# Kernel tuning notes

Measured on AMD Instinct MI355X. Metric: run time of the kernel, lower is better.

Reference implementation:

```python
import jax, jax.numpy as jnp
import numpy as np

T = 16384
D_IN = 512
D_HID = 512
D_OUT = 512


def setup_inputs() -> dict:
    key = jax.random.key(0)
    ks = jax.random.split(key, 7)
    s_in = 1.0 / np.sqrt(D_IN)
    s_hid = 1.0 / np.sqrt(D_HID)
    xs = jax.random.normal(ks[0], (T, D_IN), dtype=jnp.float32)
    Wz = jax.random.uniform(ks[1], (D_HID, D_IN), jnp.float32, -s_in, s_in)
    bz = jax.random.uniform(ks[2], (D_HID,), jnp.float32, -s_in, s_in)
    Wh = jax.random.uniform(ks[3], (D_HID, D_IN), jnp.float32, -s_in, s_in)
    bh = jax.random.uniform(ks[4], (D_HID,), jnp.float32, -s_in, s_in)
    Wo = jax.random.uniform(ks[5], (D_OUT, D_HID), jnp.float32, -s_hid, s_hid)
    bo = jax.random.uniform(ks[6], (D_OUT,), jnp.float32, -s_hid, s_hid)
    return {"xs": xs, "Wz": Wz, "bz": bz, "Wh": Wh, "bh": bh, "Wo": Wo, "bo": bo}


def _combine(first, second):
    a0, b0 = first
    a1, b1 = second
    return (a0 * a1, a1 * b0 + b1)


def reference(xs, Wz, bz, Wh, bh, Wo, bo):
    # gates and candidate hidden states: [T, H]
    zs = jax.nn.sigmoid(xs @ Wz.T + bz)
    hs = xs @ Wh.T + bh
    # prepend identity element (a=1, b=0) for the h_0 = 0 initial state
    a = jnp.concatenate([jnp.ones((1, zs.shape[1]), zs.dtype), 1.0 - zs], axis=0)
    b = jnp.concatenate([jnp.zeros((1, zs.shape[1]), zs.dtype), zs * hs], axis=0)
    _, states = jax.lax.associative_scan(_combine, (a, b))  # [T+1, H]
    return states[1:] @ Wo.T + bo  # [T, D_OUT]
```

## Files before the change

### kernel.cpp

```cpp
#include <hip/hip_runtime.h>
#include <hip/hip_bf16.h>
#include <cstdint>
#include <cmath>

#define T_SEQ 16384
#define DMODEL 512
#define NCHUNK 512
#define LCHUNK 32
#define W_N    (DMODEL * DMODEL)
#define N4_W   (W_N / 4)
#define N4_W3  (3 * N4_W)
#define N4_X   (T_SEQ * DMODEL / 4)
#define N4_ALL (N4_W3 + N4_X)
#define NTILE  8

typedef __bf16 bf16x8 __attribute__((ext_vector_type(8)));
typedef float  f32x4  __attribute__((ext_vector_type(4)));

using bf16 = __hip_bfloat16;

__device__ __forceinline__ void load_lds16(const void* g, void* l) {
    __builtin_amdgcn_global_load_lds((const __attribute__((address_space(1))) void*)g,
                                     (__attribute__((address_space(3))) void*)l,
                                     16, 0, 0);
}

__device__ __forceinline__ unsigned short f2bf(float f) {
    union { float f; unsigned u; } v; v.f = f;
    const unsigned r = (v.u + 0x7FFFu + ((v.u >> 16) & 1u)) >> 16;
    return (unsigned short)r;
}
__device__ __forceinline__ float bf2f(unsigned short u) {
    union { unsigned u; float f; } v; v.u = ((unsigned)u) << 16;
    return v.f;
}

__device__ __forceinline__ void comb(float& A, float& B, float fA, float fB,
                                     float sA, float sB) {
    A = fA * sA;
    B = sA * fB + sB;
}

__global__ __launch_bounds__(256) void k_convert(
    const float* __restrict__ xs,
    const float* __restrict__ Wz, const float* __restrict__ Wh,
    const float* __restrict__ Wo,
    bf16* __restrict__ xs_c, bf16* __restrict__ Wz_c,
    bf16* __restrict__ Wh_c, bf16* __restrict__ Wo_c)
{
    const int i = blockIdx.x * 256 + threadIdx.x;
    if (i >= N4_ALL) return;
    const float* src; bf16* dst; int o;
    if (i < N4_W3) {
        const int w = i >> 16; o = i & 65535;
        src = (w == 0) ? Wz : (w == 1) ? Wh : Wo;
        dst = (w == 0) ? Wz_c : (w == 1) ? Wh_c : Wo_c;
    } else {
        o = i - N4_W3; src = xs; dst = xs_c;
    }
    const float4 v = ((const float4*)src)[o];
    ushort4 r;
    r.x = f2bf(v.x); r.y = f2bf(v.y); r.z = f2bf(v.z); r.w = f2bf(v.w);
    ((ushort4*)dst)[o] = r;
}

__global__ __launch_bounds__(512, 2) void gemm_zh(
    const bf16* __restrict__ xs_c, const bf16* __restrict__ Wz, const float* __restrict__ bz,
    const bf16* __restrict__ Wh, const float* __restrict__ bh,
    unsigned int* __restrict__ ab_ws,
    float* __restrict__ ABagg)
{
    __shared__ __bf16 As[2][2][256 * 32];
    __shared__ __bf16 Zs[2][2][128 * 32];
    __shared__ __bf16 Hs[2][2][128 * 32];

    const int tid  = threadIdx.x;
    const int bm   = blockIdx.x;
    const int bn   = blockIdx.y;
    const int lane = tid & 63;
    const int wave = tid >> 6;
    const int wm   = wave >> 1;
    const int wn   = wave & 1;
    const int quad = lane >> 4;
    const int col  = lane & 15;

    f32x4 accz[4][4], acch[4][4];
    #pragma unroll
    for (int i = 0; i < 4; ++i)
        #pragma unroll
        for (int j = 0; j < 4; ++j) {
            accz[i][j] = (f32x4){0.f, 0.f, 0.f, 0.f};
            acch[i][j] = (f32x4){0.f, 0.f, 0.f, 0.f};
        }

    const int srow = tid >> 2;
    const int wq   = (tid & 3) ^ ((tid >> 3) & 3);
    const bf16* ag = xs_c + (size_t)(bm * 256 + srow) * DMODEL + wq * 8;
    const bf16* zg = Wz   + (size_t)(bn * 128 + srow) * DMODEL + wq * 8;
    const bf16* hg = Wh   + (size_t)(bn * 128 + srow) * DMODEL + wq * 8;

    const int fq = quad ^ ((col >> 1) & 3);
    int offA[4], offB[4];
    #pragma unroll
    for (int i = 0; i < 4; ++i) {
        offA[i] = (wm * 64 + i * 16 + col) * 32 + fq * 8;
        offB[i] = (wn * 64 + i * 16 + col) * 32 + fq * 8;
    }

    auto STAGE_HALF = [&](int t, int h) {
        const int b  = t & 1;
        const int ko = t * 64 + h * 32;
        load_lds16(ag + ko,                          &As[b][h][tid * 8]);
        load_lds16(ag + (size_t)128 * DMODEL + ko,   &As[b][h][(512 + tid) * 8]);
        load_lds16(zg + ko,                          &Zs[b][h][tid * 8]);
        load_lds16(hg + ko,                          &Hs[b][h][tid * 8]);
    };

    STAGE_HALF(0, 0); STAGE_HALF(0, 1);

    #pragma unroll
    for (int t = 0; t < NTILE; ++t) {
        const int b = t & 1;
        bf16x8 af[4], zf[4], hf[4];

        asm volatile("s_waitcnt vmcnt(4)" ::: "memory");
        __builtin_amdgcn_s_barrier();
        __builtin_amdgcn_sched_barrier(0);
        if (t + 1 < NTILE) STAGE_HALF(t + 1, 0);
        #pragma unroll
        for (int i = 0; i < 4; ++i) {
            af[i] = *(const bf16x8*)&As[b][0][offA[i]];
            zf[i] = *(const bf16x8*)&Zs[b][0][offB[i]];
        }
        __builtin_amdgcn_s_setprio(1);
        #pragma unroll
        for (int i = 0; i < 4; ++i)
            #pragma unroll
            for (int j = 0; j < 4; ++j)
                accz[i][j] = __builtin_amdgcn_mfma_f32_16x16x32_bf16(af[i], zf[j], accz[i][j], 0, 0, 0);
        __builtin_amdgcn_s_setprio(0);

        #pragma unroll
        for (int j = 0; j < 4; ++j)
            hf[j] = *(const bf16x8*)&Hs[b][0][offB[j]];
        __builtin_amdgcn_s_setprio(1);
        #pragma unroll
        for (int i = 0; i < 4; ++i)
            #pragma unroll
            for (int j = 0; j < 4; ++j)
                acch[i][j] = __builtin_amdgcn_mfma_f32_16x16x32_bf16(af[i], hf[j], acch[i][j], 0, 0, 0);
        __builtin_amdgcn_s_setprio(0);

        if (t + 1 < NTILE) {
            asm volatile("s_waitcnt vmcnt(4)" ::: "memory");
        } else {
            asm volatile("s_waitcnt vmcnt(0)" ::: "memory");
        }
        __builtin_amdgcn_s_barrier();
        __builtin_amdgcn_sched_barrier(0);
        if (t + 1 < NTILE) STAGE_HALF(t + 1, 1);
        #pragma unroll
        for (int i = 0; i < 4; ++i) {
            af[i] = *(const bf16x8*)&As[b][1][offA[i]];
            zf[i] = *(const bf16x8*)&Zs[b][1][offB[i]];
        }
        __builtin_amdgcn_s_setprio(1);
        #pragma unroll
        for (int i = 0; i < 4; ++i)
            #pragma unroll
            for (int j = 0; j < 4; ++j)
                accz[i][j] = __builtin_amdgcn_mfma_f32_16x16x32_bf16(af[i], zf[j], accz[i][j], 0, 0, 0);
        __builtin_amdgcn_s_setprio(0);

        #pragma unroll
        for (int j = 0; j < 4; ++j)
            hf[j] = *(const bf16x8*)&Hs[b][1][offB[j]];
        __builtin_amdgcn_s_setprio(1);
        #pragma unroll
        for (int i = 0; i < 4; ++i)
            #pragma unroll
            for (int j = 0; j < 4; ++j)
                acch[i][j] = __builtin_amdgcn_mfma_f32_16x16x32_bf16(af[i], hf[j], acch[i][j], 0, 0, 0);
        __builtin_amdgcn_s_setprio(0);
    }

    const int c_lo = bm * 8 + wm * 2;
    #pragma unroll
    for (int j = 0; j < 4; ++j) {
        const int n = bn * 128 + wn * 64 + j * 16 + col;
        const float bzv = bz[n];
        const float bhv = bh[n];
        float cA[4], cB[4];
        #pragma unroll
        for (int i = 0; i < 4; ++i) {
            const int mbase = bm * 256 + wm * 64 + i * 16 + quad * 4;
            float A = 1.f, B = 0.f;
            #pragma unroll
            for (int r = 0; r < 4; ++r) {
                const float zpre = accz[i][j][r] + bzv;
                const float hpre = acch[i][j][r] + bhv;
                const float z = 1.f / (1.f + __expf(-zpre));
                const float a = 1.f - z;
                const float b = z * hpre;
                const size_t idx = (size_t)(mbase + r) * DMODEL + n;
                ab_ws[idx] = (unsigned)f2bf(a) | ((unsigned)f2bf(b) << 16);
                A = a * A;
                B = a * B + b;
            }
            cA[i] = A; cB[i] = B;
        }
        #pragma unroll
        for (int i = 0; i < 4; ++i) {
            float pA = __shfl_xor(cA[i], 16);
            float pB = __shfl_xor(cB[i], 16);
            const bool hi1 = quad & 1;
            comb(cA[i], cB[i], hi1 ? pA : cA[i], hi1 ? pB : cB[i],
                               hi1 ? cA[i] : pA, hi1 ? cB[i] : pB);
            pA = __shfl_xor(cA[i], 32);
            pB = __shfl_xor(cB[i], 32);
            const bool hi2 = quad >> 1;
            comb(cA[i], cB[i], hi2 ? pA : cA[i], hi2 ? pB : cB[i],
                               hi2 ? cA[i] : pA, hi2 ? cB[i] : pB);
        }
        float Alo, Blo, Ahi, Bhi;
        comb(Alo, Blo, cA[0], cB[0], cA[1], cB[1]);
        comb(Ahi, Bhi, cA[2], cB[2], cA[3], cB[3]);
        if (quad == 0) {
            *(float4*)&ABagg[((size_t)n * NCHUNK + c_lo) * 2] =
                make_float4(Alo, Blo, Ahi, Bhi);
        }
    }
}

__global__ __launch_bounds__(512) void scan_p2(
    const float* __restrict__ ABagg, float* __restrict__ HpreT)
{
    const int h = blockIdx.x;
    const int c = threadIdx.x;
    __shared__ float sA[NCHUNK], sB[NCHUNK];

    const float2 v = ((const float2*)ABagg)[(size_t)h * NCHUNK + c];
    float A = v.x;
    float B = v.y;
    sA[c] = A; sB[c] = B;
    __syncthreads();

    for (int off = 1; off < NCHUNK; off <<= 1) {
        float pA = 1.f, pB = 0.f;
        if (c >= off) { pA = sA[c - off]; pB = sB[c - off]; }
        __syncthreads();
        const float nB = A * pB + B;
        const float nA = A * pA;
        A = nA; B = nB;
        sA[c] = A; sB[c] = B;
        __syncthreads();
    }
    const float hp = (c == 0) ? 0.f : sB[c - 1];
    HpreT[(size_t)h * NCHUNK + c] = hp;
}

__global__ __launch_bounds__(256) void scan_p3(
    const unsigned int* __restrict__ ab_ws, const float* __restrict__ HpreT,
    unsigned short* __restrict__ states)
{
    const int tid = threadIdx.x;
    const int c   = blockIdx.x;
    const int ch  = blockIdx.y * 256 + tid;
    float H = HpreT[(size_t)ch * NCHUNK + c];
    const size_t base = (size_t)(c * LCHUNK) * DMODEL + ch;
    #pragma unroll 8
    for (int i = 0; i < LCHUNK; ++i) {
        const unsigned u = ab_ws[base + (size_t)i * DMODEL];
        const float a = bf2f((unsigned short)(u & 0xFFFFu));
        const float b = bf2f((unsigned short)(u >> 16));
        H = a * H + b;
        states[base + (size_t)i * DMODEL] = f2bf(H);
    }
}

__global__ __launch_bounds__(512, 2) void gemm_out(
    const bf16* __restrict__ states, const bf16* __restrict__ Wo, const float* __restrict__ bo,
    float* __restrict__ out)
{
    __shared__ __bf16 As[2][2][256 * 32];
    __shared__ __bf16 Bs[2][2][128 * 32];

    const int tid  = threadIdx.x;
    const int bm   = blockIdx.x;
    const int bn   = blockIdx.y;
    const int lane = tid & 63;
    const int wave = tid >> 6;
    const int wm   = wave >> 1;
    const int wn   = wave & 1;
    const int quad = lane >> 4;
    const int col  = lane & 15;

    f32x4 acc[4][4];
    #pragma unroll
    for (int i = 0; i < 4; ++i)
        #pragma unroll
        for (int j = 0; j < 4; ++j)
            acc[i][j] = (f32x4){0.f, 0.f, 0.f, 0.f};

    const int srow = tid >> 2;
    const int wq   = (tid & 3) ^ ((tid >> 3) & 3);
    const bf16* ag = states + (size_t)(bm * 256 + srow) * DMODEL + wq * 8;
    const bf16* bg = Wo     + (size_t)(bn * 128 + srow) * DMODEL + wq * 8;

    const int fq = quad ^ ((col >> 1) & 3);
    int offA[4], offB[4];
    #pragma unroll
    for (int i = 0; i < 4; ++i) {
        offA[i] = (wm * 64 + i * 16 + col) * 32 + fq * 8;
        offB[i] = (wn * 64 + i * 16 + col) * 32 + fq * 8;
    }

    auto STAGE_HALF = [&](int t, int h) {
        const int b  = t & 1;
        const int ko = t * 64 + h * 32;
        load_lds16(ag + ko,                        &As[b][h][tid * 8]);
        load_lds16(ag + (size_t)128 * DMODEL + ko, &As[b][h][(512 + tid) * 8]);
        load_lds16(bg + ko,                        &Bs[b][h][tid * 8]);
    };

    STAGE_HALF(0, 0); STAGE_HALF(0, 1);

    #pragma unroll
    for (int t = 0; t < NTILE; ++t) {
        const int b = t & 1;
        bf16x8 af[4], bf[4];

        asm volatile("s_waitcnt vmcnt(3)" ::: "memory");
        __builtin_amdgcn_s_barrier();
        __builtin_amdgcn_sched_barrier(0);
        if (t + 1 < NTILE) STAGE_HALF(t + 1, 0);
        #pragma unroll
        for (int i = 0; i < 4; ++i) {
            af[i] = *(const bf16x8*)&As[b][0][offA[i]];
            bf[i] = *(const bf16x8*)&Bs[b][0][offB[i]];
        }
        __builtin_amdgcn_s_setprio(1);
        #pragma unroll
        for (int i = 0; i < 4; ++i)
            #pragma unroll
            for (int j = 0; j < 4; ++j)
                acc[i][j] = __builtin_amdgcn_mfma_f32_16x16x32_bf16(af[i], bf[j], acc[i][j], 0, 0, 0);
        __builtin_amdgcn_s_setprio(0);

        if (t + 1 < NTILE) {
            asm volatile("s_waitcnt vmcnt(3)" ::: "memory");
        } else {
            asm volatile("s_waitcnt vmcnt(0)" ::: "memory");
        }
        __builtin_amdgcn_s_barrier();
        __builtin_amdgcn_sched_barrier(0);
        if (t + 1 < NTILE) STAGE_HALF(t + 1, 1);
        #pragma unroll
        for (int i = 0; i < 4; ++i) {
            af[i] = *(const bf16x8*)&As[b][1][offA[i]];
            bf[i] = *(const bf16x8*)&Bs[b][1][offB[i]];
        }
        __builtin_amdgcn_s_setprio(1);
        #pragma unroll
        for (int i = 0; i < 4; ++i)
            #pragma unroll
            for (int j = 0; j < 4; ++j)
                acc[i][j] = __builtin_amdgcn_mfma_f32_16x16x32_bf16(af[i], bf[j], acc[i][j], 0, 0, 0);
        __builtin_amdgcn_s_setprio(0);
    }

    #pragma unroll
    for (int j = 0; j < 4; ++j) {
        const int n = bn * 128 + wn * 64 + j * 16 + col;
        const float bov = bo[n];
        #pragma unroll
        for (int i = 0; i < 4; ++i) {
            const int mbase = bm * 256 + wm * 64 + i * 16 + quad * 4;
            #pragma unroll
            for (int r = 0; r < 4; ++r)
                out[(size_t)(mbase + r) * DMODEL + n] = acc[i][j][r] + bov;
        }
    }
}

extern "C" void kernel_launch(void* const* d_in, const int* in_sizes, int n_in,
                              void* d_out, int out_size, void* d_ws, size_t ws_size,
                              hipStream_t stream)
{
    const float* xs = (const float*)d_in[0];
    const float* Wz = (const float*)d_in[1];
    const float* bz = (const float*)d_in[2];
    const float* Wh = (const float*)d_in[3];
    const float* bh = (const float*)d_in[4];
    const float* Wo = (const float*)d_in[5];
    const float* bo = (const float*)d_in[6];
    float* out = (float*)d_out;

    char* w = (char*)d_ws;
    unsigned int* ab_ws = (unsigned int*)(w);
    bf16*  xs_c   = (bf16*) (w + 33554432ull);
    bf16*  Wz_c   = (bf16*) (w + 50331648ull);
    bf16*  Wh_c   = (bf16*) (w + 50855936ull);
    bf16*  Wo_c   = (bf16*) (w + 51380224ull);
    float* ABagg  = (float*)(w + 51904512ull);
    float* HpreT  = (float*)(w + 54001664ull);
    unsigned short* states = (unsigned short*)xs_c;

    k_convert<<<(N4_ALL + 255) / 256, 256, 0, stream>>>(xs, Wz, Wh, Wo, xs_c, Wz_c, Wh_c, Wo_c);
    gemm_zh<<<dim3(64, 4), 512, 0, stream>>>(xs_c, Wz_c, bz, Wh_c, bh, ab_ws, ABagg);
    scan_p2<<<DMODEL, NCHUNK, 0, stream>>>(ABagg, HpreT);
    scan_p3<<<dim3(NCHUNK, 2), 256, 0, stream>>>(ab_ws, HpreT, states);
    gemm_out<<<dim3(64, 4), 512, 0, stream>>>((const bf16*)states, Wo_c, bo, out);
}
```

Before: 148.2 us.

## Fuse xs fp32-to-bf16 conversion into gemm_zh with triple-buffered fp32 staging

Drops the separate pass that converts xs to bf16. gemm_zh now stages fp32 xs tiles straight into LDS and packs them to bf16 fragments in registers. This saves a full read and write of the 32MB-fp32 activation through HBM. In exchange the pipeline moves from double-buffered 64-wide K tiles to triple-buffered 32-wide K steps. The doubled A bytes in LDS and the removed occupancy hint (launch_bounds 512,2 to 512) may lower occupancy and add conversion ALU work inside the main loop.

```diff
diff --git a/kernel.cpp b/kernel.cpp
--- a/kernel.cpp
+++ b/kernel.cpp
@@ -10,9 +10,8 @@
 #define W_N    (DMODEL * DMODEL)
 #define N4_W   (W_N / 4)
 #define N4_W3  (3 * N4_W)
-#define N4_X   (T_SEQ * DMODEL / 4)
-#define N4_ALL (N4_W3 + N4_X)
 #define NTILE  8
+#define NHS    16
 
 typedef __bf16 bf16x8 __attribute__((ext_vector_type(8)));
 typedef float  f32x4  __attribute__((ext_vector_type(4)));
@@ -35,6 +34,17 @@
     return v.f;
 }
 
+__device__ __forceinline__ bf16x8 packfrag(const f32x4 lo, const f32x4 hi) {
+    __hip_bfloat162 p0 = __float22bfloat162_rn(make_float2(lo[0], lo[1]));
+    __hip_bfloat162 p1 = __float22bfloat162_rn(make_float2(lo[2], lo[3]));
+    __hip_bfloat162 p2 = __float22bfloat162_rn(make_float2(hi[0], hi[1]));
+    __hip_bfloat162 p3 = __float22bfloat162_rn(make_float2(hi[2], hi[3]));
+    union { unsigned u[4]; bf16x8 v; } r;
+    r.u[0] = *(const unsigned*)&p0; r.u[1] = *(const unsigned*)&p1;
+    r.u[2] = *(const unsigned*)&p2; r.u[3] = *(const unsigned*)&p3;
+    return r.v;
+}
+
 __device__ __forceinline__ void comb(float& A, float& B, float fA, float fB,
                                      float sA, float sB) {
     A = fA * sA;
@@ -42,37 +52,31 @@
 }
 
 __global__ __launch_bounds__(256) void k_convert(
-    const float* __restrict__ xs,
     const float* __restrict__ Wz, const float* __restrict__ Wh,
     const float* __restrict__ Wo,
-    bf16* __restrict__ xs_c, bf16* __restrict__ Wz_c,
-    bf16* __restrict__ Wh_c, bf16* __restrict__ Wo_c)
+    bf16* __restrict__ Wz_c, bf16* __restrict__ Wh_c, bf16* __restrict__ Wo_c)
 {
     const int i = blockIdx.x * 256 + threadIdx.x;
-    if (i >= N4_ALL) return;
-    const float* src; bf16* dst; int o;
-    if (i < N4_W3) {
-        const int w = i >> 16; o = i & 65535;
-        src = (w == 0) ? Wz : (w == 1) ? Wh : Wo;
-        dst = (w == 0) ? Wz_c : (w == 1) ? Wh_c : Wo_c;
-    } else {
-        o = i - N4_W3; src = xs; dst = xs_c;
-    }
+    if (i >= N4_W3) return;
+    const int w = i >> 16;
+    const int o = i & 65535;
+    const float* src = (w == 0) ? Wz : (w == 1) ? Wh : Wo;
+    bf16* dst = (w == 0) ? Wz_c : (w == 1) ? Wh_c : Wo_c;
     const float4 v = ((const float4*)src)[o];
     ushort4 r;
     r.x = f2bf(v.x); r.y = f2bf(v.y); r.z = f2bf(v.z); r.w = f2bf(v.w);
     ((ushort4*)dst)[o] = r;
 }
 
-__global__ __launch_bounds__(512, 2) void gemm_zh(
-    const bf16* __restrict__ xs_c, const bf16* __restrict__ Wz, const float* __restrict__ bz,
+__global__ __launch_bounds__(512) void gemm_zh(
+    const float* __restrict__ xs, const bf16* __restrict__ Wz, const float* __restrict__ bz,
     const bf16* __restrict__ Wh, const float* __restrict__ bh,
     unsigned int* __restrict__ ab_ws,
     float* __restrict__ ABagg)
 {
-    __shared__ __bf16 As[2][2][256 * 32];
-    __shared__ __bf16 Zs[2][2][128 * 32];
-    __shared__ __bf16 Hs[2][2][128 * 32];
+    __shared__ float  Af[3][256 * 32];
+    __shared__ __bf16 Zs[3][128 * 32];
+    __shared__ __bf16 Hs[3][128 * 32];
 
     const int tid  = threadIdx.x;
     const int bm   = blockIdx.x;
@@ -93,45 +97,63 @@
             acch[i][j] = (f32x4){0.f, 0.f, 0.f, 0.f};
         }
 
-    const int srow = tid >> 2;
+    const int arow0 = tid >> 3;
+    const int aslot = (tid & 7) ^ ((tid >> 3) & 7);
+    const float* ag = xs + (size_t)(bm * 256 + arow0) * DMODEL + aslot * 4;
+
+    const int wrow = tid >> 2;
     const int wq   = (tid & 3) ^ ((tid >> 3) & 3);
-    const bf16* ag = xs_c + (size_t)(bm * 256 + srow) * DMODEL + wq * 8;
-    const bf16* zg = Wz   + (size_t)(bn * 128 + srow) * DMODEL + wq * 8;
-    const bf16* hg = Wh   + (size_t)(bn * 128 + srow) * DMODEL + wq * 8;
-
+    const bf16* zg = Wz + (size_t)(bn * 128 + wrow) * DMODEL + wq * 8;
+    const bf16* hg = Wh + (size_t)(bn * 128 + wrow) * DMODEL + wq * 8;
+
+    const int akey = col & 7;
+    int aoffL[4], aoffH[4];
+    #pragma unroll
+    for (int i = 0; i < 4; ++i) {
+        const int base = (wm * 64 + i * 16 + col) * 32;
+        aoffL[i] = base + ((2 * quad)     ^ akey) * 4;
+        aoffH[i] = base + ((2 * quad + 1) ^ akey) * 4;
+    }
     const int fq = quad ^ ((col >> 1) & 3);
-    int offA[4], offB[4];
-    #pragma unroll
-    for (int i = 0; i < 4; ++i) {
-        offA[i] = (wm * 64 + i * 16 + col) * 32 + fq * 8;
-        offB[i] = (wn * 64 + i * 16 + col) * 32 + fq * 8;
-    }
-
-    auto STAGE_HALF = [&](int t, int h) {
-        const int b  = t & 1;
-        const int ko = t * 64 + h * 32;
-        load_lds16(ag + ko,                          &As[b][h][tid * 8]);
-        load_lds16(ag + (size_t)128 * DMODEL + ko,   &As[b][h][(512 + tid) * 8]);
-        load_lds16(zg + ko,                          &Zs[b][h][tid * 8]);
-        load_lds16(hg + ko,                          &Hs[b][h][tid * 8]);
+    int offB[4];
+    #pragma unroll
+    for (int j = 0; j < 4; ++j)
+        offB[j] = (wn * 64 + j * 16 + col) * 32 + fq * 8;
+
+    auto STAGE = [&](int s, int p) {
+        const int k0 = s * 32;
+        #pragma unroll
+        for (int it = 0; it < 4; ++it)
+            load_lds16(ag + (size_t)(it * 64) * DMODEL + k0,
+                       &Af[p][(it * 512 + tid) * 4]);
+        load_lds16(zg + k0, &Zs[p][tid * 8]);
+        load_lds16(hg + k0, &Hs[p][tid * 8]);
     };
 
-    STAGE_HALF(0, 0); STAGE_HALF(0, 1);
-
-    #pragma unroll
-    for (int t = 0; t < NTILE; ++t) {
-        const int b = t & 1;
-        bf16x8 af[4], zf[4], hf[4];
-
-        asm volatile("s_waitcnt vmcnt(4)" ::: "memory");
+    STAGE(0, 0); STAGE(1, 1);
+
+    #pragma unroll
+    for (int s = 0; s < NHS; ++s) {
+        const int p = s % 3;
+        if (s + 1 < NHS) {
+            asm volatile("s_waitcnt vmcnt(6)" ::: "memory");
+        } else {
+            asm volatile("s_waitcnt vmcnt(0)" ::: "memory");
+        }
         __builtin_amdgcn_s_barrier();
         __builtin_amdgcn_sched_barrier(0);
-        if (t + 1 < NTILE) STAGE_HALF(t + 1, 0);
-        #pragma unroll
-        for (int i = 0; i < 4; ++i) {
-            af[i] = *(const bf16x8*)&As[b][0][offA[i]];
-            zf[i] = *(const bf16x8*)&Zs[b][0][offB[i]];
-        }
+        if (s + 2 < NHS) STAGE(s + 2, (s + 2) % 3);
+
+        bf16x8 af[4], zf[4], hf[4];
+        #pragma unroll
+        for (int i = 0; i < 4; ++i) {
+            const f32x4 lo = *(const f32x4*)&Af[p][aoffL[i]];
+            const f32x4 hi = *(const f32x4*)&Af[p][aoffH[i]];
+            af[i] = packfrag(lo, hi);
+        }
+        #pragma unroll
+        for (int j = 0; j < 4; ++j)
+            zf[j] = *(const bf16x8*)&Zs[p][offB[j]];
         __builtin_amdgcn_s_setprio(1);
         #pragma unroll
         for (int i = 0; i < 4; ++i)
@@ -142,39 +164,7 @@
 
         #pragma unroll
         for (int j = 0; j < 4; ++j)
-            hf[j] = *(const bf16x8*)&Hs[b][0][offB[j]];
-        __builtin_amdgcn_s_setprio(1);
-        #pragma unroll
-        for (int i = 0; i < 4; ++i)
-            #pragma unroll
-            for (int j = 0; j < 4; ++j)
-                acch[i][j] = __builtin_amdgcn_mfma_f32_16x16x32_bf16(af[i], hf[j], acch[i][j], 0, 0, 0);
-        __builtin_amdgcn_s_setprio(0);
-
-        if (t + 1 < NTILE) {
-            asm volatile("s_waitcnt vmcnt(4)" ::: "memory");
-        } else {
-            asm volatile("s_waitcnt vmcnt(0)" ::: "memory");
-        }
-        __builtin_amdgcn_s_barrier();
-        __builtin_amdgcn_sched_barrier(0);
-        if (t + 1 < NTILE) STAGE_HALF(t + 1, 1);
-        #pragma unroll
-        for (int i = 0; i < 4; ++i) {
-            af[i] = *(const bf16x8*)&As[b][1][offA[i]];
-            zf[i] = *(const bf16x8*)&Zs[b][1][offB[i]];
-        }
-        __builtin_amdgcn_s_setprio(1);
-        #pragma unroll
-        for (int i = 0; i < 4; ++i)
-            #pragma unroll
-            for (int j = 0; j < 4; ++j)
-                accz[i][j] = __builtin_amdgcn_mfma_f32_16x16x32_bf16(af[i], zf[j], accz[i][j], 0, 0, 0);
-        __builtin_amdgcn_s_setprio(0);
-
-        #pragma unroll
-        for (int j = 0; j < 4; ++j)
-            hf[j] = *(const bf16x8*)&Hs[b][1][offB[j]];
+            hf[j] = *(const bf16x8*)&Hs[p][offB[j]];
         __builtin_amdgcn_s_setprio(1);
         #pragma unroll
         for (int i = 0; i < 4; ++i)
@@ -397,17 +387,16 @@
     float* out = (float*)d_out;
 
     char* w = (char*)d_ws;
-    unsigned int* ab_ws = (unsigned int*)(w);
-    bf16*  xs_c   = (bf16*) (w + 33554432ull);
+    unsigned int*   ab_ws  = (unsigned int*)  (w);
+    unsigned short* states = (unsigned short*)(w + 33554432ull);
     bf16*  Wz_c   = (bf16*) (w + 50331648ull);
     bf16*  Wh_c   = (bf16*) (w + 50855936ull);
     bf16*  Wo_c   = (bf16*) (w + 51380224ull);
     float* ABagg  = (float*)(w + 51904512ull);
     float* HpreT  = (float*)(w + 54001664ull);
-    unsigned short* states = (unsigned short*)xs_c;
-
-    k_convert<<<(N4_ALL + 255) / 256, 256, 0, stream>>>(xs, Wz, Wh, Wo, xs_c, Wz_c, Wh_c, Wo_c);
-    gemm_zh<<<dim3(64, 4), 512, 0, stream>>>(xs_c, Wz_c, bz, Wh_c, bh, ab_ws, ABagg);
+
+    k_convert<<<(N4_W3 + 255) / 256, 256, 0, stream>>>(Wz, Wh, Wo, Wz_c, Wh_c, Wo_c);
+    gemm_zh<<<dim3(64, 4), 512, 0, stream>>>(xs, Wz_c, bz, Wh_c, bh, ab_ws, ABagg);
     scan_p2<<<DMODEL, NCHUNK, 0, stream>>>(ABagg, HpreT);
     scan_p3<<<dim3(NCHUNK, 2), 256, 0, stream>>>(ab_ws, HpreT, states);
     gemm_out<<<dim3(64, 4), 512, 0, stream>>>((const bf16*)states, Wo_c, bo, out);
```

Measured after the change: 154.8 us. +4.5%, slower.
